# Optimization experiments

Hardware: AMD Instinct MI355X
Metric: run time of the kernel (lower is better)

## Reference

```python
import jax, jax.numpy as jnp
import numpy as np

HEADS = 16
NEG_INF = -1e30


def rel_shift(t):
    # t: [b, h, i, j] with i == j; Transformer-XL style relative shift
    b, h, i, j = t.shape
    t = jnp.pad(t, ((0, 0), (0, 0), (0, 0), (1, 0)))  # zero pad on last dim front
    t = t.reshape(b, h, j + 1, i)[:, :, 1:]
    return t.reshape(b, h, i, j)


def setup_inputs() -> dict:
    key = jax.random.key(0)
    ks = jax.random.split(key, 8)
    b, n, dim = 2, 2048, 1024
    d_head = dim // HEADS
    w = 0.02
    return {
        "x": jax.random.normal(ks[0], (b, n, dim), dtype=jnp.float32),
        "pos_emb": jax.random.normal(ks[1], (n, dim), dtype=jnp.float32),
        "Wq": jax.random.normal(ks[2], (dim, dim), dtype=jnp.float32) * w,
        "bq": jnp.zeros((dim,), dtype=jnp.float32),
        "Wkv": jax.random.normal(ks[3], (dim, 2 * dim), dtype=jnp.float32) * w,
        "bkv": jnp.zeros((2 * dim,), dtype=jnp.float32),
        "Wp": jax.random.normal(ks[4], (dim, d_head), dtype=jnp.float32) * w,
        "bp": jnp.zeros((d_head,), dtype=jnp.float32),
        "Wo": jax.random.normal(ks[5], (dim, dim), dtype=jnp.float32) * w,
        "bo": jnp.zeros((dim,), dtype=jnp.float32),
    }


def reference(x, pos_emb, Wq, bq, Wkv, bkv, Wp, bp, Wo, bo):
    b, n, dim = x.shape
    h = HEADS
    d = dim // h
    scale = d ** -0.5

    q = (x @ Wq + bq).reshape(b, n, h, d).transpose(0, 2, 1, 3)  # b h n d
    kv = x @ Wkv + bkv
    k, v = jnp.split(kv, 2, axis=-1)
    k = k.reshape(b, n, h, d).transpose(0, 2, 1, 3)
    v = v.reshape(b, n, h, d).transpose(0, 2, 1, 3)

    dots = jnp.einsum('bhid,bhjd->bhij', q, k) * scale

    # relative position bias
    p = pos_emb @ Wp + bp  # [n, d]
    pos_attn = jnp.einsum('bhid,jd->bhij', q, p) * scale
    dots = dots + rel_shift(pos_attn)

    # causal mask
    causal = jnp.triu(jnp.ones((n, n), dtype=bool), 1)
    dots = jnp.where(causal[None, None], NEG_INF, dots)

    attn = jax.nn.softmax(dots, axis=-1)
    out = jnp.einsum('bhij,bhjd->bhid', attn, v)
    out = out.transpose(0, 2, 1, 3).reshape(b, n, dim)
    return out @ Wo + bo
```

## Files before the change

### kernel.cpp

```cpp
#include <hip/hip_runtime.h>
#include <hip/hip_bf16.h>
#include <cstdint>
#include <cstddef>

#define SEQ_N 2048
#define DIM   1024
#define NHEAD 16
#define DH    64

typedef __bf16 bf16;
typedef __attribute__((ext_vector_type(8))) __bf16 bf16x8;
typedef __attribute__((ext_vector_type(4))) __bf16 bf16x4;
typedef __attribute__((ext_vector_type(4))) float f32x4;

__device__ __forceinline__ void gl_lds16(const bf16* g, bf16* l) {
    __builtin_amdgcn_global_load_lds(
        (const __attribute__((address_space(1))) unsigned int*)g,
        (__attribute__((address_space(3))) unsigned int*)l, 16, 0, 0);
}

__global__ __launch_bounds__(256) void prep_kernel(
    const float* __restrict__ x, const float* __restrict__ pos,
    const float* __restrict__ Wq, const float* __restrict__ Wkv,
    const float* __restrict__ Wo, const float* __restrict__ Wp,
    bf16* __restrict__ xb, bf16* __restrict__ posb,
    bf16* __restrict__ WqkvT, bf16* __restrict__ WoT, bf16* __restrict__ WpT)
{
    int bid = blockIdx.x;
    if (bid < 6144) {
        const int NX = 4096 * 1024;
        int i = (bid * 256 + threadIdx.x) * 4;
        if (i < NX) {
            float4 v = *(const float4*)&x[i];
            xb[i + 0] = (bf16)v.x; xb[i + 1] = (bf16)v.y;
            xb[i + 2] = (bf16)v.z; xb[i + 3] = (bf16)v.w;
        } else {
            int j = i - NX;
            float4 v = *(const float4*)&pos[j];
            posb[j + 0] = (bf16)v.x; posb[j + 1] = (bf16)v.y;
            posb[j + 2] = (bf16)v.z; posb[j + 3] = (bf16)v.w;
        }
        return;
    }
    __shared__ float t[32][33];
    bid -= 6144;
    const float* src; bf16* dst; int tidx, nx, N;
    if (bid < 1024)      { src = Wq;  dst = WqkvT;                       tidx = bid;        nx = 32; N = 1024; }
    else if (bid < 3072) { src = Wkv; dst = WqkvT + (size_t)1024 * 1024; tidx = bid - 1024; nx = 64; N = 2048; }
    else if (bid < 4096) { src = Wo;  dst = WoT;                         tidx = bid - 3072; nx = 32; N = 1024; }
    else                 { src = Wp;  dst = WpT;                         tidx = bid - 4096; nx = 2;  N = 64;   }
    int n0 = (tidx % nx) * 32, k0 = (tidx / nx) * 32;
    int tx = threadIdx.x & 31, ty = threadIdx.x >> 5;
    #pragma unroll
    for (int r = ty; r < 32; r += 8)
        t[r][tx] = src[(size_t)(k0 + r) * N + n0 + tx];
    __syncthreads();
    #pragma unroll
    for (int r = ty; r < 32; r += 8)
        dst[(size_t)(n0 + r) * 1024 + k0 + tx] = (bf16)t[tx][r];
}

__global__ __launch_bounds__(256) void qkvp_kernel(
    const bf16* __restrict__ xb, const bf16* __restrict__ WqkvT,
    const bf16* __restrict__ posb, const bf16* __restrict__ WpT,
    const float* __restrict__ bq, const float* __restrict__ bkv,
    const float* __restrict__ bp,
    bf16* __restrict__ qbuf, bf16* __restrict__ kbuf,
    bf16* __restrict__ vtbuf, bf16* __restrict__ pfrag)
{
    __shared__ __align__(16) bf16 sm[128 * 132];
    bf16* At = sm;
    bf16* Bt = sm + 128 * 64;
    const int tid = threadIdx.x, w = tid >> 6, lane = tid & 63;
    const int q = lane >> 4, ln15 = lane & 15;
    const int lr = lane >> 3, c_log = (lane & 7) ^ lr;
    const int bx = blockIdx.x, by = blockIdx.y;
    const int m0 = by * 128;

    if (bx == 24) {
        if (by >= 16) return;
        f32x4 acc[2][4] = {};
        for (int k0 = 0; k0 < 1024; k0 += 64) {
            __syncthreads();
            #pragma unroll
            for (int t = 0; t < 4; ++t)
                gl_lds16(&posb[(size_t)(m0 + 32 * w + 8 * t + lr) * 1024 + k0 + c_log * 8],
                         &At[(32 * w + 8 * t) * 64]);
            #pragma unroll
            for (int t = 0; t < 2; ++t)
                gl_lds16(&WpT[(size_t)(16 * w + 8 * t + lr) * 1024 + k0 + c_log * 8],
                         &Bt[(16 * w + 8 * t) * 64]);
            __syncthreads();
            bf16x8 bfr[2][4];
            #pragma unroll
            for (int ks = 0; ks < 2; ++ks)
                #pragma unroll
                for (int sn = 0; sn < 4; ++sn) {
                    int rb = 16 * sn + ln15;
                    bfr[ks][sn] = *(const bf16x8*)&Bt[(rb * 8 + ((4 * ks + q) ^ (rb & 7))) * 8];
                }
            #pragma unroll
            for (int sm2 = 0; sm2 < 2; ++sm2) {
                int ra = 32 * w + 16 * sm2 + ln15;
                #pragma unroll
                for (int ks = 0; ks < 2; ++ks) {
                    bf16x8 af = *(const bf16x8*)&At[(ra * 8 + ((4 * ks + q) ^ (ra & 7))) * 8];
                    #pragma unroll
                    for (int sn = 0; sn < 4; ++sn)
                        acc[sm2][sn] = __builtin_amdgcn_mfma_f32_16x16x32_bf16(
                            af, bfr[ks][sn], acc[sm2][sn], 0, 0, 0);
                }
            }
        }
        #pragma unroll
        for (int sm2 = 0; sm2 < 2; ++sm2)
            #pragma unroll
            for (int sn = 0; sn < 4; ++sn)
                #pragma unroll
                for (int r = 0; r < 4; ++r) {
                    int row = m0 + 32 * w + 16 * sm2 + 4 * q + r;
                    int d = 16 * sn + ln15;
                    int sb = row >> 4, lnp = row & 15;
                    int ks2 = d >> 5, qd = (d >> 3) & 3, e = d & 7;
                    pfrag[(((size_t)sb * 2 + ks2) * 64 + qd * 16 + lnp) * 8 + e] =
                        (bf16)(acc[sm2][sn][r] + bp[d]);
                }
        return;
    }

    const int n0 = bx * 128;
    const int wm = w >> 1, wn = w & 1;
    f32x4 acc[4][4] = {};

    for (int k0 = 0; k0 < 1024; k0 += 64) {
        __syncthreads();
        #pragma unroll
        for (int t = 0; t < 4; ++t) {
            int r = 32 * w + 8 * t + lr;
            gl_lds16(&xb[(size_t)(m0 + r) * 1024 + k0 + c_log * 8],
                     &At[(32 * w + 8 * t) * 64]);
            gl_lds16(&WqkvT[(size_t)(n0 + r) * 1024 + k0 + c_log * 8],
                     &Bt[(32 * w + 8 * t) * 64]);
        }
        __syncthreads();

        bf16x8 af[2][4], bfr[2][4];
        #pragma unroll
        for (int ks = 0; ks < 2; ++ks)
            #pragma unroll
            for (int s = 0; s < 4; ++s) {
                int ra = 64 * wm + 16 * s + ln15;
                af[ks][s]  = *(const bf16x8*)&At[(ra * 8 + ((4 * ks + q) ^ (ra & 7))) * 8];
                int rb = 64 * wn + 16 * s + ln15;
                bfr[ks][s] = *(const bf16x8*)&Bt[(rb * 8 + ((4 * ks + q) ^ (rb & 7))) * 8];
            }
        #pragma unroll
        for (int ks = 0; ks < 2; ++ks)
            #pragma unroll
            for (int si = 0; si < 4; ++si)
                #pragma unroll
                for (int sj = 0; sj < 4; ++sj)
                    acc[si][sj] = __builtin_amdgcn_mfma_f32_16x16x32_bf16(
                        af[ks][si], bfr[ks][sj], acc[si][sj], 0, 0, 0);
    }

    if (bx < 16) {
        #pragma unroll
        for (int si = 0; si < 4; ++si)
            #pragma unroll
            for (int sj = 0; sj < 4; ++sj)
                #pragma unroll
                for (int r = 0; r < 4; ++r) {
                    int row = m0 + 64 * wm + 16 * si + 4 * q + r;
                    int col = n0 + 64 * wn + 16 * sj + ln15;
                    float v = acc[si][sj][r] + (col < 1024 ? bq[col] : bkv[col - 1024]);
                    if (col < 1024) qbuf[(size_t)row * 1024 + col] = (bf16)v;
                    else            kbuf[(size_t)row * 1024 + (col - 1024)] = (bf16)v;
                }
    } else {
        __syncthreads();
        #pragma unroll
        for (int si = 0; si < 4; ++si)
            #pragma unroll
            for (int sj = 0; sj < 4; ++sj) {
                int dL = 64 * wn + 16 * sj + ln15;
                int tL = 64 * wm + 16 * si + 4 * q;
                float bias = bkv[1024 + (bx - 16) * 128 + dL];
                bf16x4 o4;
                #pragma unroll
                for (int r = 0; r < 4; ++r)
                    o4[r] = (bf16)(acc[si][sj][r] + bias);
                *(bf16x4*)&sm[dL * 132 + tL] = o4;
            }
        __syncthreads();
        const int b = m0 >> 11;
        const int t0 = m0 & 2047;
        const int h0 = (bx - 16) * 2;
        #pragma unroll
        for (int p = 0; p < 16; ++p) {
            int d = (tid >> 5) + 8 * p;
            int t = (tid & 31) * 4;
            bf16x4 v4 = *(const bf16x4*)&sm[d * 132 + t];
            int rowv = (b * NHEAD + h0 + (d >> 6)) * DH + (d & 63);
            *(bf16x4*)&vtbuf[(size_t)rowv * SEQ_N + t0 + t] = v4;
        }
    }
}

__global__ __launch_bounds__(256, 4) void attn_mfma_kernel(
    const bf16* __restrict__ qb,
    const bf16* __restrict__ kb,
    const bf16* __restrict__ vt,
    const bf16* __restrict__ pfrag,
    bf16* __restrict__ ob)
{
    const int f    = (int)blockIdx.x + ((int)blockIdx.y << 5);
    const int slot = f >> 3;
    const int bh   = ((f & 7) << 2) + (slot & 3);
    const int bi   = bh >> 4, hh = bh & 15;
    const int g    = (slot >> 2) & 7;
    const int pass = slot >> 5;
    const int qblk = (pass == 0) ? g
                   : (pass == 1) ? 15 - g
                   : (pass == 2) ? 16 + g
                   :               31 - g;
    const int i0 = qblk << 6;
    const int tid = threadIdx.x, w = tid >> 6, lane = tid & 63;
    const int q = lane >> 4, ln15 = lane & 15;
    const int lr = lane >> 3, c_log = (lane & 7) ^ lr;

    __shared__ __align__(16) bf16 smem[17664];
    bf16* Ks  = smem;
    bf16* Vs  = smem + 4096;
    bf16* S2L = smem + 8192 + w * 1344;
    bf16* Pw  = smem + 13568 + w * 1024;

    const bf16* qbase = qb + ((size_t)(bi * SEQ_N + i0)) * DIM + hh * DH;
    const bf16* kbase = kb + ((size_t)bi * SEQ_N) * DIM + hh * DH;
    const bf16* vbase = vt + ((size_t)(bi * NHEAD + hh) * DH) * SEQ_N;

    bf16x8 kreg[2], vreg[2];
    #pragma unroll
    for (int t = 0; t < 2; ++t) {
        int r = 16 * w + 8 * t + lr;
        kreg[t] = *(const bf16x8*)&kbase[(size_t)r * DIM + c_log * 8];
        vreg[t] = *(const bf16x8*)&vbase[(size_t)r * SEQ_N + c_log * 8];
    }
    bf16x8 qf0 = *(const bf16x8*)&qbase[(size_t)(16 * w + ln15) * DIM + q * 8];
    bf16x8 qf1 = *(const bf16x8*)&qbase[(size_t)(16 * w + ln15) * DIM + 32 + q * 8];

    const int A0 = 127 - 4 * qblk - w;
    f32x4 s2r4;
    {
        bf16x8 f0 = *(const bf16x8*)&pfrag[(((size_t)A0 * 2 + 0) * 64 + lane) * 8];
        bf16x8 f1 = *(const bf16x8*)&pfrag[(((size_t)A0 * 2 + 1) * 64 + lane) * 8];
        f32x4 a = {0.f, 0.f, 0.f, 0.f};
        a = __builtin_amdgcn_mfma_f32_16x16x32_bf16(f0, qf0, a, 0, 0, 0);
        a = __builtin_amdgcn_mfma_f32_16x16x32_bf16(f1, qf1, a, 0, 0, 0);
        s2r4 = a;
    }
    {
        f32x4 s2r[5];
        s2r[0] = s2r4;
        #pragma unroll
        for (int s = 1; s <= 4; ++s) {
            int sb = A0 + s; if (sb > 127) sb = 127;
            bf16x8 f0 = *(const bf16x8*)&pfrag[(((size_t)sb * 2 + 0) * 64 + lane) * 8];
            bf16x8 f1 = *(const bf16x8*)&pfrag[(((size_t)sb * 2 + 1) * 64 + lane) * 8];
            f32x4 a = {0.f, 0.f, 0.f, 0.f};
            a = __builtin_amdgcn_mfma_f32_16x16x32_bf16(f0, qf0, a, 0, 0, 0);
            a = __builtin_amdgcn_mfma_f32_16x16x32_bf16(f1, qf1, a, 0, 0, 0);
            s2r[s] = a;
        }
        s2r4 = s2r[4];
        #pragma unroll
        for (int s = 0; s < 5; ++s)
            #pragma unroll
            for (int r = 0; r < 4; ++r)
                S2L[ln15 * 84 + 16 * s + 4 * q + r] = (bf16)s2r[s][r];
    }
    #pragma unroll
    for (int t = 0; t < 2; ++t) {
        *(bf16x8*)&Ks[(16 * w + 8 * t) * 64 + lane * 8] = kreg[t];
        *(bf16x8*)&Vs[(16 * w + 8 * t) * 64 + lane * 8] = vreg[t];
    }
    asm volatile("s_waitcnt lgkmcnt(0)\n\ts_barrier" ::: "memory");
    {
        int jl = (qblk > 0) ? 1 : 0;
        int j0n = jl << 6;
        #pragma unroll
        for (int t = 0; t < 2; ++t) {
            int r = 16 * w + 8 * t + lr;
            kreg[t] = *(const bf16x8*)&kbase[(size_t)(j0n + r) * DIM + c_log * 8];
            vreg[t] = *(const bf16x8*)&vbase[(size_t)r * SEQ_N + j0n + c_log * 8];
        }
    }

    const float SCL = 0.125f * 1.44269504088896341f;
    float m_run = -1e30f, l_run = 0.f;
    f32x4 O_T[4] = {};

    for (int jt = 0; ; ++jt) {
        const bool doS2 = (jt < qblk);

        float sv[4][4];
        __builtin_amdgcn_s_setprio(1);
        #pragma unroll
        for (int sn = 0; sn < 4; ++sn) {
            int rk = 16 * sn + ln15;
            bf16x8 k0f = *(const bf16x8*)&Ks[(rk * 8 + ((q    ) ^ (rk & 7))) * 8];
            bf16x8 k1f = *(const bf16x8*)&Ks[(rk * 8 + ((4 + q) ^ (rk & 7))) * 8];
            f32x4 a = {0.f, 0.f, 0.f, 0.f};
            a = __builtin_amdgcn_mfma_f32_16x16x32_bf16(k0f, qf0, a, 0, 0, 0);
            a = __builtin_amdgcn_mfma_f32_16x16x32_bf16(k1f, qf1, a, 0, 0, 0);
            #pragma unroll
            for (int r = 0; r < 4; ++r) {
                int jl = 16 * sn + 4 * q + r;
                float b = (float)S2L[ln15 * 84 + 15 - ln15 + jl];
                sv[sn][r] = (a[r] + b) * SCL;
            }
        }
        __builtin_amdgcn_s_setprio(0);
        if (jt == qblk) {
            #pragma unroll
            for (int sn = 0; sn < 4; ++sn)
                #pragma unroll
                for (int r = 0; r < 4; ++r)
                    if (16 * sn + 4 * q + r > 16 * w + ln15)
                        sv[sn][r] = -1e30f;
        }

        float mx = sv[0][0];
        #pragma unroll
        for (int sn = 0; sn < 4; ++sn)
            #pragma unroll
            for (int r = 0; r < 4; ++r)
                mx = fmaxf(mx, sv[sn][r]);
        mx = fmaxf(mx, __shfl_xor(mx, 16));
        mx = fmaxf(mx, __shfl_xor(mx, 32));
        const float mn = fmaxf(m_run, mx);
        float sum = 0.f;
        #pragma unroll
        for (int sn = 0; sn < 4; ++sn)
            #pragma unroll
            for (int r = 0; r < 4; ++r) {
                float e = exp2f(sv[sn][r] - mn);
                sv[sn][r] = e;
                sum += e;
            }
        sum += __shfl_xor(sum, 16);
        sum += __shfl_xor(sum, 32);
        const float alpha = exp2f(m_run - mn);
        l_run = l_run * alpha + sum;
        m_run = mn;

        if (doS2) {
            f32x4 s2r[5];
            s2r[0] = s2r4;
            #pragma unroll
            for (int s = 1; s <= 4; ++s) {
                int sb = A0 + 4 * (jt + 1) + s;
                if (sb > 127) sb = 127;
                bf16x8 f0 = *(const bf16x8*)&pfrag[(((size_t)sb * 2 + 0) * 64 + lane) * 8];
                bf16x8 f1 = *(const bf16x8*)&pfrag[(((size_t)sb * 2 + 1) * 64 + lane) * 8];
                f32x4 a = {0.f, 0.f, 0.f, 0.f};
                a = __builtin_amdgcn_mfma_f32_16x16x32_bf16(f0, qf0, a, 0, 0, 0);
                a = __builtin_amdgcn_mfma_f32_16x16x32_bf16(f1, qf1, a, 0, 0, 0);
                s2r[s] = a;
            }
            s2r4 = s2r[4];
            #pragma unroll
            for (int s = 0; s < 5; ++s)
                #pragma unroll
                for (int r = 0; r < 4; ++r)
                    S2L[ln15 * 84 + 16 * s + 4 * q + r] = (bf16)s2r[s][r];
        }

        #pragma unroll
        for (int sn = 0; sn < 4; ++sn)
            #pragma unroll
            for (int r = 0; r < 4; ++r) {
                int chunk = (2 * sn + (q >> 1)) ^ (ln15 & 7);
                Pw[ln15 * 64 + chunk * 8 + 4 * (q & 1) + r] = (bf16)sv[sn][r];
            }
        #pragma unroll
        for (int sd = 0; sd < 4; ++sd)
            #pragma unroll
            for (int r = 0; r < 4; ++r)
                O_T[sd][r] *= alpha;

        __builtin_amdgcn_s_setprio(1);
        #pragma unroll
        for (int ks = 0; ks < 2; ++ks) {
            bf16x8 pT = *(const bf16x8*)&Pw[ln15 * 64 + (((4 * ks + q) ^ (ln15 & 7))) * 8];
            #pragma unroll
            for (int sd = 0; sd < 4; ++sd) {
                int rv = 16 * sd + ln15;
                bf16x8 vf = *(const bf16x8*)&Vs[(rv * 8 + ((4 * ks + q) ^ (rv & 7))) * 8];
                O_T[sd] = __builtin_amdgcn_mfma_f32_16x16x32_bf16(vf, pT, O_T[sd], 0, 0, 0);
            }
        }
        __builtin_amdgcn_s_setprio(0);

        if (jt == qblk) break;

        asm volatile("s_waitcnt lgkmcnt(0)\n\ts_barrier" ::: "memory");

        #pragma unroll
        for (int t = 0; t < 2; ++t) {
            *(bf16x8*)&Ks[(16 * w + 8 * t) * 64 + lane * 8] = kreg[t];
            *(bf16x8*)&Vs[(16 * w + 8 * t) * 64 + lane * 8] = vreg[t];
        }

        {
            int jl2 = (jt + 2 <= qblk) ? jt + 2 : qblk;
            int j0n = jl2 << 6;
            #pragma unroll
            for (int t = 0; t < 2; ++t) {
                int r = 16 * w + 8 * t + lr;
                kreg[t] = *(const bf16x8*)&kbase[(size_t)(j0n + r) * DIM + c_log * 8];
                vreg[t] = *(const bf16x8*)&vbase[(size_t)r * SEQ_N + j0n + c_log * 8];
            }
        }

        asm volatile("s_waitcnt lgkmcnt(0)\n\ts_barrier" ::: "memory");
    }

    const float inv = 1.0f / l_run;
    const size_t row = (size_t)bi * SEQ_N + i0 + 16 * w + ln15;
    #pragma unroll
    for (int sd = 0; sd < 4; ++sd) {
        bf16x4 o4;
        #pragma unroll
        for (int r = 0; r < 4; ++r)
            o4[r] = (bf16)(O_T[sd][r] * inv);
        *(bf16x4*)&ob[row * DIM + hh * DH + 16 * sd + 4 * q] = o4;
    }
}

__global__ __launch_bounds__(256) void outproj_kernel(
    const bf16* __restrict__ ab, const bf16* __restrict__ WoT,
    const float* __restrict__ bo, float* __restrict__ out)
{
    __shared__ __align__(16) bf16 At[128 * 64];
    __shared__ __align__(16) bf16 Bt[64 * 64];
    const int tid = threadIdx.x, w = tid >> 6, lane = tid & 63;
    const int q = lane >> 4, ln15 = lane & 15;
    const int lr = lane >> 3, c_log = (lane & 7) ^ lr;
    const int m0 = blockIdx.y * 128, n0 = blockIdx.x * 64;

    f32x4 acc[2][4] = {};
    for (int k0 = 0; k0 < 1024; k0 += 64) {
        __syncthreads();
        #pragma unroll
        for (int t = 0; t < 4; ++t)
            gl_lds16(&ab[(size_t)(m0 + 32 * w + 8 * t + lr) * 1024 + k0 + c_log * 8],
                     &At[(32 * w + 8 * t) * 64]);
        #pragma unroll
        for (int t = 0; t < 2; ++t)
            gl_lds16(&WoT[(size_t)(n0 + 16 * w + 8 * t + lr) * 1024 + k0 + c_log * 8],
                     &Bt[(16 * w + 8 * t) * 64]);
        __syncthreads();

        bf16x8 bfr[2][4];
        #pragma unroll
        for (int ks = 0; ks < 2; ++ks)
            #pragma unroll
            for (int sn = 0; sn < 4; ++sn) {
                int rb = 16 * sn + ln15;
                bfr[ks][sn] = *(const bf16x8*)&Bt[(rb * 8 + ((4 * ks + q) ^ (rb & 7))) * 8];
            }
        #pragma unroll
        for (int sm2 = 0; sm2 < 2; ++sm2) {
            int ra = 32 * w + 16 * sm2 + ln15;
            #pragma unroll
            for (int ks = 0; ks < 2; ++ks) {
                bf16x8 af = *(const bf16x8*)&At[(ra * 8 + ((4 * ks + q) ^ (ra & 7))) * 8];
                #pragma unroll
                for (int sn = 0; sn < 4; ++sn)
                    acc[sm2][sn] = __builtin_amdgcn_mfma_f32_16x16x32_bf16(
                        af, bfr[ks][sn], acc[sm2][sn], 0, 0, 0);
            }
        }
    }
    #pragma unroll
    for (int sm2 = 0; sm2 < 2; ++sm2)
        #pragma unroll
        for (int sn = 0; sn < 4; ++sn) {
            int col = n0 + 16 * sn + ln15;
            float bias = bo[col];
            #pragma unroll
            for (int r = 0; r < 4; ++r) {
                int row = m0 + 32 * w + 16 * sm2 + 4 * q + r;
                out[(size_t)row * 1024 + col] = acc[sm2][sn][r] + bias;
            }
        }
}

extern "C" void kernel_launch(void* const* d_in, const int* in_sizes, int n_in,
                              void* d_out, int out_size, void* d_ws, size_t ws_size,
                              hipStream_t stream)
{
    const float* x    = (const float*)d_in[0];
    const float* pos  = (const float*)d_in[1];
    const float* Wq   = (const float*)d_in[2];
    const float* bq   = (const float*)d_in[3];
    const float* Wkv  = (const float*)d_in[4];
    const float* bkv  = (const float*)d_in[5];
    const float* Wp   = (const float*)d_in[6];
    const float* bp   = (const float*)d_in[7];
    const float* Wo   = (const float*)d_in[8];
    const float* bo   = (const float*)d_in[9];
    float* out = (float*)d_out;

    const int M = 2 * SEQ_N;
    char* ws = (char*)d_ws;
    bf16* xb     = (bf16*)ws;  ws += (size_t)M * DIM * 2;
    bf16* posb   = (bf16*)ws;  ws += (size_t)SEQ_N * DIM * 2;
    bf16* WqkvT  = (bf16*)ws;  ws += (size_t)3072 * 1024 * 2;
    bf16* WoT    = (bf16*)ws;  ws += (size_t)DIM * DIM * 2;
    bf16* WpT    = (bf16*)ws;  ws += (size_t)DH * DIM * 2;
    bf16* qbuf   = (bf16*)ws;  ws += (size_t)M * DIM * 2;
    bf16* kbuf   = (bf16*)ws;  ws += (size_t)M * DIM * 2;
    bf16* vtbuf  = (bf16*)ws;  ws += (size_t)M * DIM * 2;
    bf16* pfrag  = (bf16*)ws;  ws += (size_t)512 * 1024;
    bf16* abuf   = (bf16*)ws;

    dim3 blk(256);
    prep_kernel<<<dim3(10304), blk, 0, stream>>>(
        x, pos, Wq, Wkv, Wo, Wp, xb, posb, WqkvT, WoT, WpT);

    qkvp_kernel<<<dim3(25, 32), blk, 0, stream>>>(
        xb, WqkvT, posb, WpT, bq, bkv, bp, qbuf, kbuf, vtbuf, pfrag);

    attn_mfma_kernel<<<dim3(32, 32), blk, 0, stream>>>(
        qbuf, kbuf, vtbuf, pfrag, abuf);

    outproj_kernel<<<dim3(16, 32), blk, 0, stream>>>(
        abuf, WoT, bo, out);
}
```

Before: 257.8 us.

## Double-buffer K via direct global-to-LDS loads and read V straight from global

Folds the softmax scale into Q during projection and seeds the QK MFMA accumulator with the positional bias, which removes per-element scale and add work. K tiles are now double-buffered in LDS using global_load_lds, replacing register staging with two barriers per step. V fragments are read directly from global memory instead of through LDS. The O rescale is skipped when no row maximum grows. The trade-off is that the V reads now depend on cache hits and global latency sits inside the PV MFMA loop. There is also a risk of a missing wait on the async LDS loads, and rounding Q to bf16 after scaling changes precision slightly.

```diff
diff --git a/kernel.cpp b/kernel.cpp
--- a/kernel.cpp
+++ b/kernel.cpp
@@ -165,6 +165,7 @@
     }
 
     if (bx < 16) {
+        const float QSCL = 0.125f * 1.44269504088896341f;
         #pragma unroll
         for (int si = 0; si < 4; ++si)
             #pragma unroll
@@ -174,7 +175,7 @@
                     int row = m0 + 64 * wm + 16 * si + 4 * q + r;
                     int col = n0 + 64 * wn + 16 * sj + ln15;
                     float v = acc[si][sj][r] + (col < 1024 ? bq[col] : bkv[col - 1024]);
-                    if (col < 1024) qbuf[(size_t)row * 1024 + col] = (bf16)v;
+                    if (col < 1024) qbuf[(size_t)row * 1024 + col] = (bf16)(v * QSCL);
                     else            kbuf[(size_t)row * 1024 + (col - 1024)] = (bf16)v;
                 }
     } else {
@@ -230,8 +231,8 @@
     const int lr = lane >> 3, c_log = (lane & 7) ^ lr;
 
     __shared__ __align__(16) bf16 smem[17664];
-    bf16* Ks  = smem;
-    bf16* Vs  = smem + 4096;
+    bf16* KsA = smem;
+    bf16* KsB = smem + 4096;
     bf16* S2L = smem + 8192 + w * 1344;
     bf16* Pw  = smem + 13568 + w * 1024;
 
@@ -239,15 +240,13 @@
     const bf16* kbase = kb + ((size_t)bi * SEQ_N) * DIM + hh * DH;
     const bf16* vbase = vt + ((size_t)(bi * NHEAD + hh) * DH) * SEQ_N;
 
-    bf16x8 kreg[2], vreg[2];
-    #pragma unroll
-    for (int t = 0; t < 2; ++t) {
-        int r = 16 * w + 8 * t + lr;
-        kreg[t] = *(const bf16x8*)&kbase[(size_t)r * DIM + c_log * 8];
-        vreg[t] = *(const bf16x8*)&vbase[(size_t)r * SEQ_N + c_log * 8];
-    }
     bf16x8 qf0 = *(const bf16x8*)&qbase[(size_t)(16 * w + ln15) * DIM + q * 8];
     bf16x8 qf1 = *(const bf16x8*)&qbase[(size_t)(16 * w + ln15) * DIM + 32 + q * 8];
+
+    #pragma unroll
+    for (int t = 0; t < 2; ++t)
+        gl_lds16(kbase + (size_t)(16 * w + 8 * t + lr) * DIM + c_log * 8,
+                 &KsA[(16 * w + 8 * t) * 64]);
 
     const int A0 = 127 - 4 * qblk - w;
     f32x4 s2r4;
@@ -279,46 +278,42 @@
             for (int r = 0; r < 4; ++r)
                 S2L[ln15 * 84 + 16 * s + 4 * q + r] = (bf16)s2r[s][r];
     }
-    #pragma unroll
-    for (int t = 0; t < 2; ++t) {
-        *(bf16x8*)&Ks[(16 * w + 8 * t) * 64 + lane * 8] = kreg[t];
-        *(bf16x8*)&Vs[(16 * w + 8 * t) * 64 + lane * 8] = vreg[t];
-    }
-    asm volatile("s_waitcnt lgkmcnt(0)\n\ts_barrier" ::: "memory");
-    {
-        int jl = (qblk > 0) ? 1 : 0;
-        int j0n = jl << 6;
-        #pragma unroll
-        for (int t = 0; t < 2; ++t) {
-            int r = 16 * w + 8 * t + lr;
-            kreg[t] = *(const bf16x8*)&kbase[(size_t)(j0n + r) * DIM + c_log * 8];
-            vreg[t] = *(const bf16x8*)&vbase[(size_t)r * SEQ_N + j0n + c_log * 8];
-        }
-    }
-
-    const float SCL = 0.125f * 1.44269504088896341f;
+    __syncthreads();
+
     float m_run = -1e30f, l_run = 0.f;
     f32x4 O_T[4] = {};
+    int cur = 0;
 
     for (int jt = 0; ; ++jt) {
+        const int j0 = jt << 6;
         const bool doS2 = (jt < qblk);
+        bf16* Kc = cur ? KsB : KsA;
+        bf16* Kn = cur ? KsA : KsB;
+
+        if (doS2) {
+            const bf16* kn = kbase + (size_t)(j0 + 64) * DIM;
+            #pragma unroll
+            for (int t = 0; t < 2; ++t)
+                gl_lds16(kn + (size_t)(16 * w + 8 * t + lr) * DIM + c_log * 8,
+                         &Kn[(16 * w + 8 * t) * 64]);
+        }
 
         float sv[4][4];
         __builtin_amdgcn_s_setprio(1);
         #pragma unroll
         for (int sn = 0; sn < 4; ++sn) {
             int rk = 16 * sn + ln15;
-            bf16x8 k0f = *(const bf16x8*)&Ks[(rk * 8 + ((q    ) ^ (rk & 7))) * 8];
-            bf16x8 k1f = *(const bf16x8*)&Ks[(rk * 8 + ((4 + q) ^ (rk & 7))) * 8];
-            f32x4 a = {0.f, 0.f, 0.f, 0.f};
+            bf16x8 k0f = *(const bf16x8*)&Kc[(rk * 8 + ((q    ) ^ (rk & 7))) * 8];
+            bf16x8 k1f = *(const bf16x8*)&Kc[(rk * 8 + ((4 + q) ^ (rk & 7))) * 8];
+            f32x4 a;
+            #pragma unroll
+            for (int r = 0; r < 4; ++r)
+                a[r] = (float)S2L[ln15 * 84 + 15 - ln15 + 16 * sn + 4 * q + r];
             a = __builtin_amdgcn_mfma_f32_16x16x32_bf16(k0f, qf0, a, 0, 0, 0);
             a = __builtin_amdgcn_mfma_f32_16x16x32_bf16(k1f, qf1, a, 0, 0, 0);
             #pragma unroll
-            for (int r = 0; r < 4; ++r) {
-                int jl = 16 * sn + 4 * q + r;
-                float b = (float)S2L[ln15 * 84 + 15 - ln15 + jl];
-                sv[sn][r] = (a[r] + b) * SCL;
-            }
+            for (int r = 0; r < 4; ++r)
+                sv[sn][r] = a[r];
         }
         __builtin_amdgcn_s_setprio(0);
         if (jt == qblk) {
@@ -350,8 +345,17 @@
             }
         sum += __shfl_xor(sum, 16);
         sum += __shfl_xor(sum, 32);
-        const float alpha = exp2f(m_run - mn);
-        l_run = l_run * alpha + sum;
+        if (__all(mx <= m_run)) {
+            l_run += sum;
+        } else {
+            const float alpha = exp2f(m_run - mn);
+            l_run = l_run * alpha + sum;
+            #pragma unroll
+            for (int sd = 0; sd < 4; ++sd)
+                #pragma unroll
+                for (int r = 0; r < 4; ++r)
+                    O_T[sd][r] *= alpha;
+        }
         m_run = mn;
 
         if (doS2) {
@@ -383,11 +387,6 @@
                 int chunk = (2 * sn + (q >> 1)) ^ (ln15 & 7);
                 Pw[ln15 * 64 + chunk * 8 + 4 * (q & 1) + r] = (bf16)sv[sn][r];
             }
-        #pragma unroll
-        for (int sd = 0; sd < 4; ++sd)
-            #pragma unroll
-            for (int r = 0; r < 4; ++r)
-                O_T[sd][r] *= alpha;
 
         __builtin_amdgcn_s_setprio(1);
         #pragma unroll
@@ -395,8 +394,8 @@
             bf16x8 pT = *(const bf16x8*)&Pw[ln15 * 64 + (((4 * ks + q) ^ (ln15 & 7))) * 8];
             #pragma unroll
             for (int sd = 0; sd < 4; ++sd) {
-                int rv = 16 * sd + ln15;
-                bf16x8 vf = *(const bf16x8*)&Vs[(rv * 8 + ((4 * ks + q) ^ (rv & 7))) * 8];
+                bf16x8 vf = *(const bf16x8*)&vbase[(size_t)(16 * sd + ln15) * SEQ_N
+                                                   + j0 + (4 * ks + q) * 8];
                 O_T[sd] = __builtin_amdgcn_mfma_f32_16x16x32_bf16(vf, pT, O_T[sd], 0, 0, 0);
             }
         }
@@ -404,26 +403,8 @@
 
         if (jt == qblk) break;
 
-        asm volatile("s_waitcnt lgkmcnt(0)\n\ts_barrier" ::: "memory");
-
-        #pragma unroll
-        for (int t = 0; t < 2; ++t) {
-            *(bf16x8*)&Ks[(16 * w + 8 * t) * 64 + lane * 8] = kreg[t];
-            *(bf16x8*)&Vs[(16 * w + 8 * t) * 64 + lane * 8] = vreg[t];
-        }
-
-        {
-            int jl2 = (jt + 2 <= qblk) ? jt + 2 : qblk;
-            int j0n = jl2 << 6;
-            #pragma unroll
-            for (int t = 0; t < 2; ++t) {
-                int r = 16 * w + 8 * t + lr;
-                kreg[t] = *(const bf16x8*)&kbase[(size_t)(j0n + r) * DIM + c_log * 8];
-                vreg[t] = *(const bf16x8*)&vbase[(size_t)r * SEQ_N + j0n + c_log * 8];
-            }
-        }
-
-        asm volatile("s_waitcnt lgkmcnt(0)\n\ts_barrier" ::: "memory");
+        __syncthreads();
+        cur ^= 1;
     }
 
     const float inv = 1.0f / l_run;
```

After: 275.1 us. 6.7% more time.
